# Kernel tuning notes

Hardware: AMD Instinct MI355X
Metric: run time of the kernel (lower is better)

Reference implementation:

```python
import jax, jax.numpy as jnp
import numpy as np

N = 100000      # number of nodes
F = 256         # input feature dim
O = 128         # output_size
NNZ_X = 1_600_000
NNZ_A = 1_600_000
KEEP_PROB = 0.9  # 1 - dropout_rate


def setup_inputs() -> dict:
    key = jax.random.key(0)
    ks = jax.random.split(key, 8)
    x_vals = jax.random.uniform(ks[0], (NNZ_X,), dtype=jnp.float32)
    kernel = jax.random.normal(ks[1], (F, O), dtype=jnp.float32) * (1.0 / np.sqrt(F))
    adj_vals = jax.random.uniform(ks[2], (NNZ_A,), dtype=jnp.float32)
    x_rows = jax.random.randint(ks[3], (NNZ_X,), 0, N, dtype=jnp.int32)
    x_cols = jax.random.randint(ks[4], (NNZ_X,), 0, F, dtype=jnp.int32)
    adj_rows = jax.random.randint(ks[5], (NNZ_A,), 0, N, dtype=jnp.int32)
    adj_cols = jax.random.randint(ks[6], (NNZ_A,), 0, N, dtype=jnp.int32)
    # dropout_sparse: floor(keep_prob + U[0,1)) -> Bernoulli(keep_prob) retain mask
    keep_mask = jax.random.uniform(ks[7], (NNZ_X,)) < KEEP_PROB
    return {"x_vals": x_vals, "kernel": kernel, "adj_vals": adj_vals,
            "x_rows": x_rows, "x_cols": x_cols,
            "adj_rows": adj_rows, "adj_cols": adj_cols,
            "keep_mask": keep_mask}


def reference(x_vals, kernel, adj_vals, x_rows, x_cols, adj_rows, adj_cols, keep_mask):
    # sparse dropout: retain entries then scale by 1/keep_prob
    v = jnp.where(keep_mask, x_vals, 0.0) * (1.0 / KEEP_PROB)
    # SpMM 1: sparse [N, F] @ dense [F, O] -> gather kernel rows, scatter-add by node
    h = jax.ops.segment_sum(v[:, None] * kernel[x_cols], x_rows, num_segments=N)  # [N, O]
    # SpMM 2: sparse adj [N, N] @ dense h [N, O]
    out = jax.ops.segment_sum(adj_vals[:, None] * h[adj_cols], adj_rows, num_segments=N)  # [N, O]
    return jax.nn.relu(out)
```

## Files before the change

### kernel.cpp

```cpp
#include <hip/hip_runtime.h>
#include <hip/hip_bf16.h>


static constexpr int O_DIM = 128;
static constexpr float KEEP_INV = 1.0f / 0.9f;
static constexpr int BUCK_BINS = 256;
static constexpr int TILE = 2048;

using half_t = _Float16;
using half2_t = _Float16 __attribute__((ext_vector_type(2)));

__global__ void detect_mask_kernel(const unsigned int* __restrict__ w, int nwords,
                                   int* __restrict__ flags) {
    __shared__ int sA[256];
    __shared__ int sB[256];
    int t = threadIdx.x;
    int violA = 0, violB = 0;
    for (int i = t; i < nwords; i += 256) {
        unsigned int x = w[i];
        violA |= (x > 1u) ? 1 : 0;
        violB |= (x != 0u && x != 0x3F800000u) ? 1 : 0;
    }
    sA[t] = violA; sB[t] = violB;
    __syncthreads();
    for (int s = 128; s > 0; s >>= 1) {
        if (t < s) { sA[t] |= sA[t + s]; sB[t] |= sB[t + s]; }
        __syncthreads();
    }
    if (t == 0) { flags[0] = sA[0]; flags[1] = sB[0]; }
}

__global__ void conv_kern_kernel(const float2* __restrict__ kern2,
                                 half2_t* __restrict__ k16, int n) {
    int i = blockIdx.x * 256 + threadIdx.x;
    if (i < n) {
        float2 v = kern2[i];
        half2_t o; o.x = (half_t)v.x; o.y = (half_t)v.y;
        k16[i] = o;
    }
}

__global__ __launch_bounds__(256) void tile_hist_kernel(
        const int* __restrict__ xr, int nnz_x,
        const int* __restrict__ ar, int nnz_a,
        int n_nodes, int nbuck, int B,
        int* __restrict__ histT) {
    __shared__ int hist[1024];
    int b = blockIdx.x, t = threadIdx.x;
    for (int k = t; k < 1024; k += 256) hist[k] = 0;
    __syncthreads();
    int tot = nnz_x + nnz_a;
    int tstart = b * TILE;
    int tend = min(tstart + TILE, tot);
    for (int i = tstart + t; i < tend; i += 256) {
        int bin = (i < nnz_x) ? xr[i] : (n_nodes + ar[i - nnz_x]);
        atomicAdd(&hist[bin >> 8], 1);
    }
    __syncthreads();
    for (int k = t; k < nbuck; k += 256)
        histT[(size_t)k * B + b] = hist[k];
}

static constexpr int SCAN_BS = 256;
static constexpr int SCAN_IPT = 8;
static constexpr int SCAN_CHUNK = SCAN_BS * SCAN_IPT;

__global__ __launch_bounds__(SCAN_BS) void scan_partial_kernel(const int* __restrict__ cnt,
                                                               int n, int* __restrict__ bsums) {
    int b = blockIdx.x, t = threadIdx.x;
    int lane = t & 63, wid = t >> 6;
    __shared__ int wsum[SCAN_BS / 64];
    int base = b * SCAN_CHUNK + t * SCAN_IPT;
    int s = 0;
    #pragma unroll
    for (int k = 0; k < SCAN_IPT; ++k) {
        int i = base + k;
        s += (i < n) ? cnt[i] : 0;
    }
    #pragma unroll
    for (int d = 1; d < 64; d <<= 1) s += __shfl_xor(s, d, 64);
    if (lane == 0) wsum[wid] = s;
    __syncthreads();
    if (t == 0) {
        int tot = 0;
        #pragma unroll
        for (int w = 0; w < SCAN_BS / 64; ++w) tot += wsum[w];
        bsums[b] = tot;
    }
}

__global__ __launch_bounds__(1024) void scan_blocksums_kernel(int* __restrict__ bsums, int nb,
                                                              int* __restrict__ sent0,
                                                              int* __restrict__ sent1) {
    __shared__ int wsum[16];
    int t = threadIdx.x, lane = t & 63, wid = t >> 6;
    int v = (t < nb) ? bsums[t] : 0;
    int s = v;
    #pragma unroll
    for (int d = 1; d < 64; d <<= 1) {
        int u = __shfl_up(s, d, 64);
        if (lane >= d) s += u;
    }
    if (lane == 63) wsum[wid] = s;
    __syncthreads();
    int woff = 0;
    for (int w = 0; w < wid; ++w) woff += wsum[w];
    if (t < nb) bsums[t] = woff + s - v;
    if (t == 1023) { int tot = woff + s; *sent0 = tot; *sent1 = tot; }
}

__global__ __launch_bounds__(SCAN_BS) void scan_final_kernel(const int* __restrict__ cnt, int n,
                                                             const int* __restrict__ bsums,
                                                             int* __restrict__ S) {
    __shared__ int wsum[SCAN_BS / 64];
    int b = blockIdx.x, t = threadIdx.x;
    int lane = t & 63, wid = t >> 6;
    int base = b * SCAN_CHUNK + t * SCAN_IPT;
    int v[SCAN_IPT];
    int tsum = 0;
    #pragma unroll
    for (int k = 0; k < SCAN_IPT; ++k) {
        int i = base + k;
        v[k] = (i < n) ? cnt[i] : 0;
        tsum += v[k];
    }
    int s = tsum;
    #pragma unroll
    for (int d = 1; d < 64; d <<= 1) {
        int u = __shfl_up(s, d, 64);
        if (lane >= d) s += u;
    }
    if (lane == 63) wsum[wid] = s;
    __syncthreads();
    int woff = 0;
    for (int w = 0; w < wid; ++w) woff += wsum[w];
    int excl = bsums[b] + woff + (s - tsum);
    #pragma unroll
    for (int k = 0; k < SCAN_IPT; ++k) {
        int i = base + k;
        if (i < n) S[i] = excl;
        excl += v[k];
    }
}

__global__ __launch_bounds__(256) void multisplit_kernel(
        const float* __restrict__ xv,
        const int* __restrict__ xr,
        const int* __restrict__ xc,
        const void* __restrict__ mask,
        const int* __restrict__ flags,
        const float* __restrict__ av,
        const int* __restrict__ ar,
        const int* __restrict__ ac,
        int nnz_x, int nnz_a, int n_nodes,
        int nbuck, int B,
        const int* __restrict__ tofs,
        int2* __restrict__ rec) {
    __shared__ int cur[1024];
    int b = blockIdx.x, t = threadIdx.x;
    for (int k = t; k < nbuck; k += 256)
        cur[k] = tofs[(size_t)k * B + b];
    __syncthreads();
    int tot = nnz_x + nnz_a;
    int tstart = b * TILE;
    int tend = min(tstart + TILE, tot);
    int f0 = flags[0], f1 = flags[1];
    for (int i = tstart + t; i < tend; i += 256) {
        int bin, col; float v;
        if (i < nnz_x) {
            bin = xr[i];
            col = xc[i];
            bool keep;
            if (f0 == 0)      keep = ((const int*)mask)[i] != 0;
            else if (f1 == 0) keep = ((const float*)mask)[i] != 0.0f;
            else              keep = ((const unsigned char*)mask)[i] != 0;
            v = keep ? xv[i] * KEEP_INV : 0.0f;
        } else {
            int e = i - nnz_x;
            bin = n_nodes + ar[e];
            col = ac[e];
            v = av[e];
        }
        int key = ((bin & (BUCK_BINS - 1)) << 17) | col;
        int pos = atomicAdd(&cur[bin >> 8], 1);
        rec[pos] = make_int2(key, __float_as_int(v));
    }
}

__global__ __launch_bounds__(256) void bucket_sort_kernel(
        const int2* __restrict__ rec,
        const int* __restrict__ tofs, int B,
        int ntot, int2* __restrict__ packed,
        int* __restrict__ S) {
    __shared__ int hist[256];
    __shared__ int cur[256];
    __shared__ int wsum[4];
    int bb = blockIdx.x, t = threadIdx.x;
    int start = tofs[(size_t)bb * B];
    int end   = tofs[(size_t)(bb + 1) * B];
    hist[t] = 0;
    __syncthreads();
    for (int i = start + t; i < end; i += 256) {
        unsigned k = (unsigned)rec[i].x;
        atomicAdd(&hist[k >> 17], 1);
    }
    __syncthreads();
    int v = hist[t];
    int lane = t & 63, wid = t >> 6;
    int s = v;
    #pragma unroll
    for (int d = 1; d < 64; d <<= 1) {
        int u = __shfl_up(s, d, 64);
        if (lane >= d) s += u;
    }
    if (lane == 63) wsum[wid] = s;
    __syncthreads();
    int woff = 0;
    for (int w = 0; w < wid; ++w) woff += wsum[w];
    int excl = woff + s - v;
    int binBase = bb << 8;
    if (binBase + t < ntot) S[binBase + t] = start + excl;
    cur[t] = start + excl;
    __syncthreads();
    for (int i = start + t; i < end; i += 256) {
        int2 e = rec[i];
        unsigned k = (unsigned)e.x;
        int pos = atomicAdd(&cur[k >> 17], 1);
        packed[pos] = make_int2((int)(k & 0x1FFFFu), e.y);
    }
}

__global__ __launch_bounds__(256) void spmm1_wave_kernel(
        const int* __restrict__ S, const int2* __restrict__ packed,
        const half2_t* __restrict__ k16, half2_t* __restrict__ h2,
        int n_rows) {
    int gid = blockIdx.x * 256 + threadIdx.x;
    int r = gid >> 6;
    if (r >= n_rows) return;
    int lane = gid & 63;
    int j = S[r], end = S[r + 1];
    float ax = 0.0f, ay = 0.0f;
    if ((j & 1) && j < end) {
        int2 e = packed[j];
        half2_t w = k16[e.x * 64 + lane];
        float v = __int_as_float(e.y);
        ax = fmaf(v, (float)w.x, ax); ay = fmaf(v, (float)w.y, ay);
        ++j;
    }
    for (; j + 8 <= end; j += 8) {
        int4 p0 = *(const int4*)(packed + j);
        int4 p1 = *(const int4*)(packed + j + 2);
        int4 p2 = *(const int4*)(packed + j + 4);
        int4 p3 = *(const int4*)(packed + j + 6);
        half2_t w0 = k16[p0.x * 64 + lane];
        half2_t w1 = k16[p0.z * 64 + lane];
        half2_t w2 = k16[p1.x * 64 + lane];
        half2_t w3 = k16[p1.z * 64 + lane];
        half2_t w4 = k16[p2.x * 64 + lane];
        half2_t w5 = k16[p2.z * 64 + lane];
        half2_t w6 = k16[p3.x * 64 + lane];
        half2_t w7 = k16[p3.z * 64 + lane];
        float v0 = __int_as_float(p0.y), v1 = __int_as_float(p0.w);
        float v2 = __int_as_float(p1.y), v3 = __int_as_float(p1.w);
        float v4 = __int_as_float(p2.y), v5 = __int_as_float(p2.w);
        float v6 = __int_as_float(p3.y), v7 = __int_as_float(p3.w);
        ax = fmaf(v0, (float)w0.x, ax); ay = fmaf(v0, (float)w0.y, ay);
        ax = fmaf(v1, (float)w1.x, ax); ay = fmaf(v1, (float)w1.y, ay);
        ax = fmaf(v2, (float)w2.x, ax); ay = fmaf(v2, (float)w2.y, ay);
        ax = fmaf(v3, (float)w3.x, ax); ay = fmaf(v3, (float)w3.y, ay);
        ax = fmaf(v4, (float)w4.x, ax); ay = fmaf(v4, (float)w4.y, ay);
        ax = fmaf(v5, (float)w5.x, ax); ay = fmaf(v5, (float)w5.y, ay);
        ax = fmaf(v6, (float)w6.x, ax); ay = fmaf(v6, (float)w6.y, ay);
        ax = fmaf(v7, (float)w7.x, ax); ay = fmaf(v7, (float)w7.y, ay);
    }
    if (j + 4 <= end) {
        int4 p0 = *(const int4*)(packed + j);
        int4 p1 = *(const int4*)(packed + j + 2);
        half2_t w0 = k16[p0.x * 64 + lane];
        half2_t w1 = k16[p0.z * 64 + lane];
        half2_t w2 = k16[p1.x * 64 + lane];
        half2_t w3 = k16[p1.z * 64 + lane];
        float v0 = __int_as_float(p0.y), v1 = __int_as_float(p0.w);
        float v2 = __int_as_float(p1.y), v3 = __int_as_float(p1.w);
        ax = fmaf(v0, (float)w0.x, ax); ay = fmaf(v0, (float)w0.y, ay);
        ax = fmaf(v1, (float)w1.x, ax); ay = fmaf(v1, (float)w1.y, ay);
        ax = fmaf(v2, (float)w2.x, ax); ay = fmaf(v2, (float)w2.y, ay);
        ax = fmaf(v3, (float)w3.x, ax); ay = fmaf(v3, (float)w3.y, ay);
        j += 4;
    }
    for (; j < end; ++j) {
        int2 e = packed[j];
        half2_t w = k16[e.x * 64 + lane];
        float v = __int_as_float(e.y);
        ax = fmaf(v, (float)w.x, ax); ay = fmaf(v, (float)w.y, ay);
    }
    half2_t o; o.x = (half_t)ax; o.y = (half_t)ay;
    h2[r * 64 + lane] = o;
}

__global__ __launch_bounds__(256) void spmm2_wave_kernel(
        const int* __restrict__ S, const int2* __restrict__ packed,
        const half2_t* __restrict__ h2, float2* __restrict__ out2,
        int n_rows) {
    int gid = blockIdx.x * 256 + threadIdx.x;
    int r = gid >> 6;
    if (r >= n_rows) return;
    int lane = gid & 63;
    int j = S[r], end = S[r + 1];
    float ax = 0.0f, ay = 0.0f;
    if ((j & 1) && j < end) {
        int2 e = packed[j];
        half2_t w = h2[e.x * 64 + lane];
        float v = __int_as_float(e.y);
        ax = fmaf(v, (float)w.x, ax); ay = fmaf(v, (float)w.y, ay);
        ++j;
    }
    for (; j + 16 <= end; j += 16) {
        int4 p0 = *(const int4*)(packed + j);
        int4 p1 = *(const int4*)(packed + j + 2);
        int4 p2 = *(const int4*)(packed + j + 4);
        int4 p3 = *(const int4*)(packed + j + 6);
        int4 p4 = *(const int4*)(packed + j + 8);
        int4 p5 = *(const int4*)(packed + j + 10);
        int4 p6 = *(const int4*)(packed + j + 12);
        int4 p7 = *(const int4*)(packed + j + 14);
        half2_t w0 = h2[p0.x * 64 + lane];
        half2_t w1 = h2[p0.z * 64 + lane];
        half2_t w2 = h2[p1.x * 64 + lane];
        half2_t w3 = h2[p1.z * 64 + lane];
        half2_t w4 = h2[p2.x * 64 + lane];
        half2_t w5 = h2[p2.z * 64 + lane];
        half2_t w6 = h2[p3.x * 64 + lane];
        half2_t w7 = h2[p3.z * 64 + lane];
        half2_t w8 = h2[p4.x * 64 + lane];
        half2_t w9 = h2[p4.z * 64 + lane];
        half2_t wa = h2[p5.x * 64 + lane];
        half2_t wb = h2[p5.z * 64 + lane];
        half2_t wc = h2[p6.x * 64 + lane];
        half2_t wd = h2[p6.z * 64 + lane];
        half2_t we = h2[p7.x * 64 + lane];
        half2_t wf = h2[p7.z * 64 + lane];
        float v0 = __int_as_float(p0.y), v1 = __int_as_float(p0.w);
        float v2 = __int_as_float(p1.y), v3 = __int_as_float(p1.w);
        float v4 = __int_as_float(p2.y), v5 = __int_as_float(p2.w);
        float v6 = __int_as_float(p3.y), v7 = __int_as_float(p3.w);
        float v8 = __int_as_float(p4.y), v9 = __int_as_float(p4.w);
        float va = __int_as_float(p5.y), vb = __int_as_float(p5.w);
        float vc = __int_as_float(p6.y), vd = __int_as_float(p6.w);
        float ve = __int_as_float(p7.y), vf = __int_as_float(p7.w);
        ax = fmaf(v0, (float)w0.x, ax); ay = fmaf(v0, (float)w0.y, ay);
        ax = fmaf(v1, (float)w1.x, ax); ay = fmaf(v1, (float)w1.y, ay);
        ax = fmaf(v2, (float)w2.x, ax); ay = fmaf(v2, (float)w2.y, ay);
        ax = fmaf(v3, (float)w3.x, ax); ay = fmaf(v3, (float)w3.y, ay);
        ax = fmaf(v4, (float)w4.x, ax); ay = fmaf(v4, (float)w4.y, ay);
        ax = fmaf(v5, (float)w5.x, ax); ay = fmaf(v5, (float)w5.y, ay);
        ax = fmaf(v6, (float)w6.x, ax); ay = fmaf(v6, (float)w6.y, ay);
        ax = fmaf(v7, (float)w7.x, ax); ay = fmaf(v7, (float)w7.y, ay);
        ax = fmaf(v8, (float)w8.x, ax); ay = fmaf(v8, (float)w8.y, ay);
        ax = fmaf(v9, (float)w9.x, ax); ay = fmaf(v9, (float)w9.y, ay);
        ax = fmaf(va, (float)wa.x, ax); ay = fmaf(va, (float)wa.y, ay);
        ax = fmaf(vb, (float)wb.x, ax); ay = fmaf(vb, (float)wb.y, ay);
        ax = fmaf(vc, (float)wc.x, ax); ay = fmaf(vc, (float)wc.y, ay);
        ax = fmaf(vd, (float)wd.x, ax); ay = fmaf(vd, (float)wd.y, ay);
        ax = fmaf(ve, (float)we.x, ax); ay = fmaf(ve, (float)we.y, ay);
        ax = fmaf(vf, (float)wf.x, ax); ay = fmaf(vf, (float)wf.y, ay);
    }
    if (j + 8 <= end) {
        int4 p0 = *(const int4*)(packed + j);
        int4 p1 = *(const int4*)(packed + j + 2);
        int4 p2 = *(const int4*)(packed + j + 4);
        int4 p3 = *(const int4*)(packed + j + 6);
        half2_t w0 = h2[p0.x * 64 + lane];
        half2_t w1 = h2[p0.z * 64 + lane];
        half2_t w2 = h2[p1.x * 64 + lane];
        half2_t w3 = h2[p1.z * 64 + lane];
        half2_t w4 = h2[p2.x * 64 + lane];
        half2_t w5 = h2[p2.z * 64 + lane];
        half2_t w6 = h2[p3.x * 64 + lane];
        half2_t w7 = h2[p3.z * 64 + lane];
        float v0 = __int_as_float(p0.y), v1 = __int_as_float(p0.w);
        float v2 = __int_as_float(p1.y), v3 = __int_as_float(p1.w);
        float v4 = __int_as_float(p2.y), v5 = __int_as_float(p2.w);
        float v6 = __int_as_float(p3.y), v7 = __int_as_float(p3.w);
        ax = fmaf(v0, (float)w0.x, ax); ay = fmaf(v0, (float)w0.y, ay);
        ax = fmaf(v1, (float)w1.x, ax); ay = fmaf(v1, (float)w1.y, ay);
        ax = fmaf(v2, (float)w2.x, ax); ay = fmaf(v2, (float)w2.y, ay);
        ax = fmaf(v3, (float)w3.x, ax); ay = fmaf(v3, (float)w3.y, ay);
        ax = fmaf(v4, (float)w4.x, ax); ay = fmaf(v4, (float)w4.y, ay);
        ax = fmaf(v5, (float)w5.x, ax); ay = fmaf(v5, (float)w5.y, ay);
        ax = fmaf(v6, (float)w6.x, ax); ay = fmaf(v6, (float)w6.y, ay);
        ax = fmaf(v7, (float)w7.x, ax); ay = fmaf(v7, (float)w7.y, ay);
        j += 8;
    }
    if (j + 4 <= end) {
        int4 p0 = *(const int4*)(packed + j);
        int4 p1 = *(const int4*)(packed + j + 2);
        half2_t w0 = h2[p0.x * 64 + lane];
        half2_t w1 = h2[p0.z * 64 + lane];
        half2_t w2 = h2[p1.x * 64 + lane];
        half2_t w3 = h2[p1.z * 64 + lane];
        float v0 = __int_as_float(p0.y), v1 = __int_as_float(p0.w);
        float v2 = __int_as_float(p1.y), v3 = __int_as_float(p1.w);
        ax = fmaf(v0, (float)w0.x, ax); ay = fmaf(v0, (float)w0.y, ay);
        ax = fmaf(v1, (float)w1.x, ax); ay = fmaf(v1, (float)w1.y, ay);
        ax = fmaf(v2, (float)w2.x, ax); ay = fmaf(v2, (float)w2.y, ay);
        ax = fmaf(v3, (float)w3.x, ax); ay = fmaf(v3, (float)w3.y, ay);
        j += 4;
    }
    for (; j < end; ++j) {
        int2 e = packed[j];
        half2_t w = h2[e.x * 64 + lane];
        float v = __int_as_float(e.y);
        ax = fmaf(v, (float)w.x, ax); ay = fmaf(v, (float)w.y, ay);
    }
    out2[r * 64 + lane] = make_float2(fmaxf(ax, 0.0f), fmaxf(ay, 0.0f));
}

__global__ void spmm1_atomic_kernel(const float* __restrict__ xv,
                                    const int* __restrict__ xr,
                                    const int* __restrict__ xc,
                                    const void* __restrict__ mask,
                                    const float* __restrict__ kern,
                                    const int* __restrict__ flags,
                                    float* __restrict__ h, int nnz) {
    long long gid = (long long)blockIdx.x * blockDim.x + threadIdx.x;
    int e = (int)(gid >> 7);
    if (e >= nnz) return;
    int o = (int)(gid & 127);
    bool keep;
    if (flags[0] == 0)      keep = ((const int*)mask)[e] != 0;
    else if (flags[1] == 0) keep = ((const float*)mask)[e] != 0.0f;
    else                    keep = ((const unsigned char*)mask)[e] != 0;
    if (!keep) return;
    atomicAdd(&h[(long long)xr[e] * O_DIM + o], xv[e] * KEEP_INV * kern[xc[e] * O_DIM + o]);
}

__global__ void spmm2_atomic_kernel(const float* __restrict__ av,
                                    const int* __restrict__ ar,
                                    const int* __restrict__ ac,
                                    const float* __restrict__ h,
                                    float* __restrict__ out, int nnz) {
    long long gid = (long long)blockIdx.x * blockDim.x + threadIdx.x;
    int e = (int)(gid >> 7);
    if (e >= nnz) return;
    int o = (int)(gid & 127);
    atomicAdd(&out[(long long)ar[e] * O_DIM + o], av[e] * h[(long long)ac[e] * O_DIM + o]);
}

__global__ void relu_kernel(float* __restrict__ out, int n4) {
    int stride = gridDim.x * blockDim.x;
    float4* p = (float4*)out;
    for (int i = blockIdx.x * blockDim.x + threadIdx.x; i < n4; i += stride) {
        float4 v = p[i];
        v.x = fmaxf(v.x, 0.0f); v.y = fmaxf(v.y, 0.0f);
        v.z = fmaxf(v.z, 0.0f); v.w = fmaxf(v.w, 0.0f);
        p[i] = v;
    }
}

static inline size_t align256(size_t x) { return (x + 255) & ~(size_t)255; }

extern "C" void kernel_launch(void* const* d_in, const int* in_sizes, int n_in,
                              void* d_out, int out_size, void* d_ws, size_t ws_size,
                              hipStream_t stream) {
    const float* x_vals   = (const float*)d_in[0];
    const float* kern     = (const float*)d_in[1];
    const float* adj_vals = (const float*)d_in[2];
    const int*   x_rows   = (const int*)d_in[3];
    const int*   x_cols   = (const int*)d_in[4];
    const int*   adj_rows = (const int*)d_in[5];
    const int*   adj_cols = (const int*)d_in[6];
    const void*  mask     = d_in[7];

    const int nnz_x = in_sizes[0];
    const int nnz_a = in_sizes[2];
    const int n_nodes = out_size / O_DIM;
    const int ntot = 2 * n_nodes;
    const int nbuck = (ntot + BUCK_BINS - 1) / BUCK_BINS;
    const long long nnz_tot = (long long)nnz_x + nnz_a;
    const int B = (int)((nnz_tot + TILE - 1) / TILE);
    const long long n_scan = (long long)nbuck * B;
    const int nb_scan = (int)((n_scan + SCAN_CHUNK - 1) / SCAN_CHUNK);

    float* out = (float*)d_out;
    char* ws = (char*)d_ws;

    size_t off = 0;
    int* flags = (int*)d_ws;            off = align256(off + 2 * sizeof(int));
    size_t o_k16 = off;                 off = align256(off + 256 * 128 * sizeof(half_t));
    size_t o_histT = off;               off = align256(off + (size_t)n_scan * 4);
    size_t o_tofs = off;                off = align256(off + ((size_t)n_scan + 1) * 4);
    size_t o_bsums = off;               off = align256(off + 4096 * 4);
    size_t o_S = off;                   off = align256(off + ((size_t)ntot + 1) * 4);
    size_t o_rec = off;                 off = align256(off + (size_t)nnz_tot * 8);
    size_t o_packed = off;              off = align256(off + (size_t)nnz_tot * 8);
    size_t o_h = off;                   off = align256(off + (size_t)n_nodes * O_DIM * sizeof(half_t));
    const bool csr_ok = (off <= ws_size) && (nbuck <= 1024) &&
                        (n_nodes <= (1 << 17)) && (nb_scan <= 1024);

    int scan_words = nnz_x / 4;
    if (scan_words > 16384) scan_words = 16384;
    detect_mask_kernel<<<1, 256, 0, stream>>>((const unsigned int*)mask, scan_words, flags);

    if (csr_ok) {
        half2_t* k16 = (half2_t*)(ws + o_k16);
        int*  histT  = (int*)(ws + o_histT);
        int*  tofs   = (int*)(ws + o_tofs);
        int*  bsums  = (int*)(ws + o_bsums);
        int*  S      = (int*)(ws + o_S);
        int2* rec    = (int2*)(ws + o_rec);
        int2* packed = (int2*)(ws + o_packed);
        half2_t* h2  = (half2_t*)(ws + o_h);

        conv_kern_kernel<<<64, 256, 0, stream>>>((const float2*)kern, k16, 16384);
        tile_hist_kernel<<<B, 256, 0, stream>>>(x_rows, nnz_x, adj_rows, nnz_a,
                                                n_nodes, nbuck, B, histT);
        scan_partial_kernel<<<nb_scan, SCAN_BS, 0, stream>>>(histT, (int)n_scan, bsums);
        scan_blocksums_kernel<<<1, 1024, 0, stream>>>(bsums, nb_scan,
                                                      &tofs[n_scan], &S[ntot]);
        scan_final_kernel<<<nb_scan, SCAN_BS, 0, stream>>>(histT, (int)n_scan, bsums, tofs);
        multisplit_kernel<<<B, 256, 0, stream>>>(x_vals, x_rows, x_cols, mask, flags,
                                                 adj_vals, adj_rows, adj_cols,
                                                 nnz_x, nnz_a, n_nodes, nbuck, B,
                                                 tofs, rec);
        bucket_sort_kernel<<<nbuck, 256, 0, stream>>>(rec, tofs, B, ntot, packed, S);
        {
            int blocks = (n_nodes * 64 + 255) / 256;
            spmm1_wave_kernel<<<blocks, 256, 0, stream>>>(S, packed, k16, h2, n_nodes);
        }
        {
            int blocks = (n_nodes * 64 + 255) / 256;
            spmm2_wave_kernel<<<blocks, 256, 0, stream>>>(S + n_nodes, packed, h2,
                                                          (float2*)out, n_nodes);
        }
    } else {
        float* h = (float*)(ws + 256);
        hipMemsetAsync(h, 0, (size_t)n_nodes * O_DIM * 4, stream);
        hipMemsetAsync(out, 0, (size_t)out_size * 4, stream);
        {
            long long threads = (long long)nnz_x * O_DIM;
            int blocks = (int)((threads + 255) / 256);
            spmm1_atomic_kernel<<<blocks, 256, 0, stream>>>(x_vals, x_rows, x_cols, mask,
                                                            kern, flags, h, nnz_x);
            threads = (long long)nnz_a * O_DIM;
            blocks = (int)((threads + 255) / 256);
            spmm2_atomic_kernel<<<blocks, 256, 0, stream>>>(adj_vals, adj_rows, adj_cols,
                                                            h, out, nnz_a);
        }
        int n4 = out_size / 4;
        int blocks = (n4 + 255) / 256; if (blocks > 2048) blocks = 2048;
        relu_kernel<<<blocks, 256, 0, stream>>>(out, n4);
    }
}
```

Measured before the change: 245.4 us.

## Pad per-tile bucket segments to aligned sizes and double histogram tile size

Result: slower. 311.6 us (+27.0%).

```diff
diff --git a/kernel.cpp b/kernel.cpp
--- a/kernel.cpp
+++ b/kernel.cpp
@@ -5,7 +5,7 @@
 static constexpr int O_DIM = 128;
 static constexpr float KEEP_INV = 1.0f / 0.9f;
 static constexpr int BUCK_BINS = 256;
-static constexpr int TILE = 2048;
+static constexpr int TILE = 4096;
 
 using half_t = _Float16;
 using half2_t = _Float16 __attribute__((ext_vector_type(2)));
@@ -43,7 +43,7 @@
 __global__ __launch_bounds__(256) void tile_hist_kernel(
         const int* __restrict__ xr, int nnz_x,
         const int* __restrict__ ar, int nnz_a,
-        int n_nodes, int nbuck, int B,
+        int n_nodes, int nbuck, int B, int pad,
         int* __restrict__ histT) {
     __shared__ int hist[1024];
     int b = blockIdx.x, t = threadIdx.x;
@@ -57,8 +57,9 @@
         atomicAdd(&hist[bin >> 8], 1);
     }
     __syncthreads();
+    int pm = pad - 1;
     for (int k = t; k < nbuck; k += 256)
-        histT[(size_t)k * B + b] = hist[k];
+        histT[(size_t)k * B + b] = (hist[k] + pm) & ~pm;
 }
 
 static constexpr int SCAN_BS = 256;
@@ -184,6 +185,14 @@
         int key = ((bin & (BUCK_BINS - 1)) << 17) | col;
         int pos = atomicAdd(&cur[bin >> 8], 1);
         rec[pos] = make_int2(key, __float_as_int(v));
+    }
+    __syncthreads();
+    int fillkey = (b & (BUCK_BINS - 1)) << 17;
+    for (int k = t; k < nbuck; k += 256) {
+        int fl = k * B + b;
+        int pe = tofs[fl + 1];
+        for (int p = cur[k]; p < pe; ++p)
+            rec[p] = make_int2(fillkey, 0);
     }
 }
 
@@ -492,10 +501,22 @@
     size_t o_tofs = off;                off = align256(off + ((size_t)n_scan + 1) * 4);
     size_t o_bsums = off;               off = align256(off + 4096 * 4);
     size_t o_S = off;                   off = align256(off + ((size_t)ntot + 1) * 4);
-    size_t o_rec = off;                 off = align256(off + (size_t)nnz_tot * 8);
-    size_t o_packed = off;              off = align256(off + (size_t)nnz_tot * 8);
     size_t o_h = off;                   off = align256(off + (size_t)n_nodes * O_DIM * sizeof(half_t));
-    const bool csr_ok = (off <= ws_size) && (nbuck <= 1024) &&
+    const size_t fixed_end = off;
+
+    int PAD = 8;
+    long long rec_cap = 0;
+    while (true) {
+        rec_cap = nnz_tot + (long long)(PAD - 1) * n_scan;
+        size_t need = fixed_end + 2 * align256((size_t)rec_cap * 8);
+        if (need <= ws_size || PAD == 1) break;
+        PAD >>= 1;
+    }
+    size_t o_rec = fixed_end;
+    size_t o_packed = o_rec + align256((size_t)rec_cap * 8);
+    size_t total_need = o_packed + align256((size_t)rec_cap * 8);
+
+    const bool csr_ok = (total_need <= ws_size) && (nbuck <= 1024) &&
                         (n_nodes <= (1 << 17)) && (nb_scan <= 1024);
 
     int scan_words = nnz_x / 4;
@@ -514,7 +535,7 @@
 
         conv_kern_kernel<<<64, 256, 0, stream>>>((const float2*)kern, k16, 16384);
         tile_hist_kernel<<<B, 256, 0, stream>>>(x_rows, nnz_x, adj_rows, nnz_a,
-                                                n_nodes, nbuck, B, histT);
+                                                n_nodes, nbuck, B, PAD, histT);
         scan_partial_kernel<<<nb_scan, SCAN_BS, 0, stream>>>(histT, (int)n_scan, bsums);
         scan_blocksums_kernel<<<1, 1024, 0, stream>>>(bsums, nb_scan,
                                                       &tofs[n_scan], &S[ntot]);
```
